# Performance work log

Hardware: AMD Instinct MI355X
Metric: run time of the kernel (lower is better)

## Reference

```python
import jax, jax.numpy as jnp
import numpy as np

HID = 128
HEADS = 8
HDIM = HID // HEADS
MLP = int(HID * 4.0)
N = 50000
E = 800000
EPS = 1e-6


def _ln(x):
    m = jnp.mean(x, axis=-1, keepdims=True)
    v = jnp.var(x, axis=-1, keepdims=True)
    return (x - m) / jnp.sqrt(v + EPS)


def _modulate(x, shift, scale):
    return x * (1 + scale) + shift


def setup_inputs() -> dict:
    key = jax.random.key(0)
    ks = jax.random.split(key, 12)
    s = lambda fan_in: 1.0 / np.sqrt(fan_in)
    return {
        "x": jax.random.normal(ks[0], (N, HID), dtype=jnp.float32),
        "edge_index": jax.random.randint(ks[1], (2, E), 0, N, dtype=jnp.int64),
        "c": jax.random.normal(ks[2], (N, HID), dtype=jnp.float32),
        "w_qkv": jax.random.normal(ks[3], (HID, 3 * HID), dtype=jnp.float32) * s(HID),
        "w_proj": jax.random.normal(ks[4], (HID, HID), dtype=jnp.float32) * s(HID),
        "b_proj": jnp.zeros((HID,), dtype=jnp.float32),
        "w_mlp1": jax.random.normal(ks[5], (HID, MLP), dtype=jnp.float32) * s(HID),
        "b_mlp1": jnp.zeros((MLP,), dtype=jnp.float32),
        "w_mlp2": jax.random.normal(ks[6], (MLP, HID), dtype=jnp.float32) * s(MLP),
        "b_mlp2": jnp.zeros((HID,), dtype=jnp.float32),
        "w_ada": jax.random.normal(ks[7], (HID, 6 * HID), dtype=jnp.float32) * s(HID),
        "b_ada": jnp.zeros((6 * HID,), dtype=jnp.float32),
    }


def _graph_attn(x, edge_index, w_qkv, w_proj, b_proj):
    n = x.shape[0]
    qkv = x @ w_qkv  # [N, 3*HID]
    q, k, v = jnp.split(qkv, 3, axis=-1)
    q = q.reshape(n, HEADS, HDIM)
    k = k.reshape(n, HEADS, HDIM)
    v = v.reshape(n, HEADS, HDIM)
    src = edge_index[0]  # j (source)
    dst = edge_index[1]  # i (destination / aggregation key)
    # per-edge attention score [E, HEADS]
    score = jnp.einsum('ehd,ehd->eh', q[dst], k[src]) / np.sqrt(HDIM)
    # segment softmax over destination node
    smax = jax.ops.segment_max(score, dst, num_segments=n)  # [N, H]
    ex = jnp.exp(score - smax[dst])
    den = jax.ops.segment_sum(ex, dst, num_segments=n)
    attn = ex / den[dst]  # [E, H]
    msg = v[src] * attn[:, :, None]  # [E, H, D]
    out = jax.ops.segment_sum(msg, dst, num_segments=n)  # [N, H, D]
    return out.reshape(n, HID) @ w_proj + b_proj


def reference(x, edge_index, c, w_qkv, w_proj, b_proj, w_mlp1, b_mlp1,
              w_mlp2, b_mlp2, w_ada, b_ada):
    mods = jax.nn.silu(c) @ w_ada + b_ada
    sh_msa, sc_msa, g_msa, sh_mlp, sc_mlp, g_mlp = jnp.split(mods, 6, axis=-1)
    x = x + g_msa * _graph_attn(_modulate(_ln(x), sh_msa, sc_msa),
                                edge_index, w_qkv, w_proj, b_proj)
    h = _modulate(_ln(x), sh_mlp, sc_mlp)
    h = jax.nn.gelu(h @ w_mlp1 + b_mlp1, approximate=True) @ w_mlp2 + b_mlp2
    return x + g_mlp * h
```

## Files before the change

kernel.cpp:

```cpp
#include <hip/hip_runtime.h>
#include <math.h>

#define N_NODES 50000
#define HIDD 128
#define HEADS 8
#define HDIM 16
#define NE 800000

using short8 = __attribute__((ext_vector_type(8))) short;
using f32x4 = __attribute__((ext_vector_type(4))) float;

__device__ __forceinline__ int load_idx(const void* ei, int is64, long long pos) {
  long long v = is64 ? ((const long long*)ei)[pos]
                     : (long long)((const int*)ei)[pos];
  unsigned uv = (unsigned)v;
  return (uv < N_NODES) ? (int)uv : 0;
}

__global__ void detect_kernel(const unsigned* __restrict__ ei_raw, int* flag) {
  __shared__ int any_nonzero;
  if (threadIdx.x == 0) any_nonzero = 0;
  __syncthreads();
  if (threadIdx.x < 128) {
    if (ei_raw[2 * threadIdx.x + 1] != 0u) atomicOr(&any_nonzero, 1);
  }
  __syncthreads();
  if (threadIdx.x == 0) *flag = any_nonzero ? 0 : 1;
}

__global__ __launch_bounds__(256) void probe_kernel(float* out, int n, float mb) {
  int i = blockIdx.x * 256 + threadIdx.x;
  if (i < n) out[i] = (i == 0) ? mb : 0.f;
}

struct ProNone {
  __device__ __forceinline__ float operator()(float v, int, int) const { return v; }
};
struct ProSilu {
  __device__ __forceinline__ float operator()(float v, int, int) const {
    return v / (1.f + __expf(-v));
  }
};
struct EpiNone {
  __device__ __forceinline__ float operator()(float a, int, int) const { return a; }
};
struct EpiBias {
  const float* b;
  __device__ __forceinline__ float operator()(float a, int, int c) const { return a + b[c]; }
};
struct EpiGelu {
  const float* b;
  __device__ __forceinline__ float operator()(float a, int, int c) const {
    float t = a + b[c];
    float u = 0.7978845608028654f * (t + 0.044715f * t * t * t);
    float au = fabsf(u);
    float e = __expf(2.f * au);
    float th = __builtin_copysignf(1.f - 2.f / (e + 1.f), u);
    return 0.5f * t * (1.f + th);
  }
};
struct EpiResGateB {
  const float* b;
  const float* xres;
  const unsigned short* gate;
  __device__ __forceinline__ float operator()(float a, int r, int c) const {
    float g = __uint_as_float((unsigned)gate[(size_t)r * 768 + c] << 16);
    return xres[(size_t)r * HIDD + c] + g * (a + b[c]);
  }
};

struct CvTab {
  int end[8];
  int src_sel[8];
  int src_off[8];
  int ldb[8];
  int n[8];
  int dst_off[8];
};
__global__ __launch_bounds__(256) void convert_all_kernel(
    const float* __restrict__ p0, const float* __restrict__ p1,
    const float* __restrict__ p2, const float* __restrict__ p3,
    const float* __restrict__ p4, CvTab t, int total,
    unsigned short* __restrict__ hi, unsigned short* __restrict__ lo) {
  int idx = blockIdx.x * 256 + threadIdx.x;
  if (idx >= total) return;
  int s = 0;
#pragma unroll
  for (int j = 0; j < 7; j++) s += (idx >= t.end[j]) ? 1 : 0;
  int local = idx - (s ? t.end[s - 1] : 0);
  int N = t.n[s];
  int k = (unsigned)local / (unsigned)N;
  int n = local - k * N;
  const float* B;
  int sel = t.src_sel[s];
  B = (sel == 0) ? p0 : (sel == 1) ? p1 : (sel == 2) ? p2 : (sel == 3) ? p3 : p4;
  float f = B[(size_t)k * t.ldb[s] + t.src_off[s] + n];
  unsigned u = __float_as_uint(f);
  unsigned short hs = (unsigned short)(u >> 16);
  float hf = __uint_as_float(u & 0xFFFF0000u);
  unsigned short ls = (unsigned short)(__float_as_uint(f - hf) >> 16);
  int lane = (((k >> 3) & 3) << 4) | (n & 15);
  int dst = t.dst_off[s] + (((k >> 5) * (N >> 4) + (n >> 4)) * 64 + lane) * 8 + (k & 7);
  hi[dst] = hs;
  lo[dst] = ls;
}

template <class Pro, class Epi, int OMODE = 0, int AMODE = 0>
__global__ __launch_bounds__(256) void gemm_direct(
    const void* __restrict__ Av, const void* __restrict__ Av2,
    const unsigned short* __restrict__ Bhi, const unsigned short* __restrict__ Blo,
    void* __restrict__ Cv, int M, int N, int K, Pro pro, Epi epi) {
  const int tid = threadIdx.x;
  const int lane = tid & 63;
  const int wv = tid >> 6;
  const int quad = lane >> 4;
  const int ln15 = lane & 15;
  const int mrow0 = blockIdx.x * 64 + wv * 16;
  const int arow = mrow0 + ln15;
  const int col0 = blockIdx.y * 128;
  const int Nt = N >> 4;
  const int ntbase = col0 >> 4;
  const bool aok = (arow < M);
  const int KB = K >> 5;
  float* C = (float*)Cv;

  f32x4 acc[8] = {};

  for (int kb = 0; kb < KB; kb++) {
    short8 ahi = {}, alo = {};
    if constexpr (AMODE == 0) {
      const float* A = (const float*)Av;
      float4 a0 = make_float4(0.f, 0.f, 0.f, 0.f), a1 = a0;
      if (aok) {
        const float* ap = A + (size_t)arow * K + kb * 32 + quad * 8;
        a0 = *(const float4*)ap;
        a1 = *(const float4*)(ap + 4);
        int cb = kb * 32 + quad * 8;
        a0.x = pro(a0.x, arow, cb + 0); a0.y = pro(a0.y, arow, cb + 1);
        a0.z = pro(a0.z, arow, cb + 2); a0.w = pro(a0.w, arow, cb + 3);
        a1.x = pro(a1.x, arow, cb + 4); a1.y = pro(a1.y, arow, cb + 5);
        a1.z = pro(a1.z, arow, cb + 6); a1.w = pro(a1.w, arow, cb + 7);
      }
      float f[8] = {a0.x, a0.y, a0.z, a0.w, a1.x, a1.y, a1.z, a1.w};
      union { unsigned u[4]; short8 v; } ch, cl;
#pragma unroll
      for (int e = 0; e < 4; e++) {
        unsigned u0 = __float_as_uint(f[2 * e]);
        unsigned u1 = __float_as_uint(f[2 * e + 1]);
        ch.u[e] = (u0 >> 16) | (u1 & 0xFFFF0000u);
        float h0 = __uint_as_float(u0 & 0xFFFF0000u);
        float h1 = __uint_as_float(u1 & 0xFFFF0000u);
        cl.u[e] = (__float_as_uint(f[2 * e] - h0) >> 16) |
                  (__float_as_uint(f[2 * e + 1] - h1) & 0xFFFF0000u);
      }
      ahi = ch.v;
      alo = cl.v;
    } else if constexpr (AMODE == 1) {
      if (aok)
        ahi = *(const short8*)((const unsigned short*)Av + (size_t)arow * K + kb * 32 + quad * 8);
    } else {
      if (aok) {
        size_t aoff = (size_t)arow * K + kb * 32 + quad * 8;
        ahi = *(const short8*)((const unsigned short*)Av + aoff);
        alo = *(const short8*)((const unsigned short*)Av2 + aoff);
      }
    }

    const unsigned short* bph = Bhi + ((size_t)(kb * Nt + ntbase) * 64 + lane) * 8;
    const unsigned short* bpl = Blo + ((size_t)(kb * Nt + ntbase) * 64 + lane) * 8;
#pragma unroll
    for (int nt = 0; nt < 8; nt++) {
      short8 bhi = *(const short8*)(bph + nt * 512);
      short8 blo = *(const short8*)(bpl + nt * 512);
      if constexpr (AMODE != 1)
        acc[nt] = __builtin_amdgcn_mfma_f32_16x16x32_bf16(alo, bhi, acc[nt], 0, 0, 0);
      acc[nt] = __builtin_amdgcn_mfma_f32_16x16x32_bf16(ahi, blo, acc[nt], 0, 0, 0);
      acc[nt] = __builtin_amdgcn_mfma_f32_16x16x32_bf16(ahi, bhi, acc[nt], 0, 0, 0);
    }
  }

#pragma unroll
  for (int nt = 0; nt < 8; nt++) {
    f32x4 a = acc[nt];
    int gc = col0 + nt * 16 + ln15;
#pragma unroll
    for (int r = 0; r < 4; r++) {
      int gr = mrow0 + quad * 4 + r;
      if (gr < M) {
        if constexpr (OMODE == 1) {
          float* crow = C + (size_t)gr * 256;
          if (gc < 128) {
            crow[gc] = a[r];
          } else {
            unsigned u = __float_as_uint(a[r]);
            unsigned rr = (u + 0x7FFFu + ((u >> 16) & 1u)) >> 16;
            unsigned short* kv = (unsigned short*)crow + 256;
            int c = gc - 128;
            int idx = (c < 128) ? (((c >> 2) << 3) + (c & 3))
                                : ((((c - 128) >> 2) << 3) + 4 + ((c - 128) & 3));
            kv[idx] = (unsigned short)rr;
          }
        } else if constexpr (OMODE == 2) {
          float v = epi(a[r], gr, gc);
          unsigned u = __float_as_uint(v);
          unsigned rr = (u + 0x7FFFu + ((u >> 16) & 1u)) >> 16;
          ((unsigned short*)Cv)[(size_t)gr * N + gc] = (unsigned short)rr;
        } else {
          C[(size_t)gr * N + gc] = epi(a[r], gr, gc);
        }
      }
    }
  }
}

__global__ __launch_bounds__(256) void ln_mod_kernel(
    const float* __restrict__ x, const unsigned* __restrict__ sa,
    unsigned* __restrict__ xh, unsigned* __restrict__ xl) {
  int wave = threadIdx.x >> 6;
  int lane = threadIdx.x & 63;
  int row = blockIdx.x * 4 + wave;
  if (row >= N_NODES) return;
  float2 v = *(const float2*)(x + (size_t)row * HIDD + lane * 2);
  float s = v.x + v.y;
  float sq = v.x * v.x + v.y * v.y;
#pragma unroll
  for (int o = 32; o >= 1; o >>= 1) {
    s += __shfl_xor(s, o);
    sq += __shfl_xor(sq, o);
  }
  float m = s * (1.f / 128.f);
  float var = sq * (1.f / 128.f) - m * m;
  float rs = rsqrtf(var + 1e-6f);
  unsigned shw = sa[(size_t)row * 384 + lane];
  unsigned scw = sa[(size_t)row * 384 + 64 + lane];
  float shx = __uint_as_float(shw << 16), shy = __uint_as_float(shw & 0xFFFF0000u);
  float scx = __uint_as_float(scw << 16), scy = __uint_as_float(scw & 0xFFFF0000u);
  float ox = (v.x - m) * rs * (1.f + scx) + shx;
  float oy = (v.y - m) * rs * (1.f + scy) + shy;
  unsigned ux = __float_as_uint(ox), uy = __float_as_uint(oy);
  unsigned hx = ux & 0xFFFF0000u, hy = uy & 0xFFFF0000u;
  unsigned lx = __float_as_uint(ox - __uint_as_float(hx));
  unsigned ly = __float_as_uint(oy - __uint_as_float(hy));
  xh[(size_t)row * 64 + lane] = (ux >> 16) | hy;
  xl[(size_t)row * 64 + lane] = (lx >> 16) | (ly & 0xFFFF0000u);
}

__global__ __launch_bounds__(256) void zero_int_kernel(int* p, int n) {
  int i = blockIdx.x * 256 + threadIdx.x;
  if (i < n) p[i] = 0;
}

__global__ __launch_bounds__(256) void hist_kernel(const void* __restrict__ ei,
                                                   const int* __restrict__ flag,
                                                   int* __restrict__ A) {
  int e = blockIdx.x * 256 + threadIdx.x;
  if (e >= NE) return;
  int dst = load_idx(ei, *flag, (long long)NE + e);
  atomicAdd(&A[dst + 1], 1);
}

__global__ __launch_bounds__(1024) void scan1_kernel(int* __restrict__ A, int n,
                                                     int* __restrict__ bsum) {
  __shared__ int buf[2][1024];
  int i = blockIdx.x * 1024 + threadIdx.x;
  int val = (i < n) ? A[i] : 0;
  int pb = 0;
  buf[0][threadIdx.x] = val;
  __syncthreads();
#pragma unroll
  for (int off = 1; off < 1024; off <<= 1) {
    int t = buf[pb][threadIdx.x];
    if ((int)threadIdx.x >= off) t += buf[pb][threadIdx.x - off];
    buf[pb ^ 1][threadIdx.x] = t;
    pb ^= 1;
    __syncthreads();
  }
  int incl = buf[pb][threadIdx.x];
  if (i < n) A[i] = incl;
  if (threadIdx.x == 1023) bsum[blockIdx.x] = incl;
}
__global__ void scan2_kernel(int* __restrict__ bsum, int nb) {
  int l = threadIdx.x;
  int v = (l < nb) ? bsum[l] : 0;
#pragma unroll
  for (int off = 1; off < 64; off <<= 1) {
    int t = __shfl_up(v, off);
    if (l >= off) v += t;
  }
  if (l < nb) bsum[l] = v;
}
__global__ __launch_bounds__(256) void scan3_kernel(int* __restrict__ A, int n,
                                                    const int* __restrict__ bsum) {
  int i = blockIdx.x * 256 + threadIdx.x;
  int b = i >> 10;
  if (i < n && b > 0) A[i] += bsum[b - 1];
}

__global__ __launch_bounds__(256) void scatter_kernel(const void* __restrict__ ei,
                                                      const int* __restrict__ flag,
                                                      int* __restrict__ A,
                                                      unsigned short* __restrict__ col) {
  int e = blockIdx.x * 256 + threadIdx.x;
  if (e >= NE) return;
  int is64 = *flag;
  int src = load_idx(ei, is64, e);
  int dst = load_idx(ei, is64, (long long)NE + e);
  int pos = atomicAdd(&A[dst], 1);
  col[pos] = (unsigned short)src;
}

__global__ __launch_bounds__(256) void node_attn_kernel(
    const int* __restrict__ A, const unsigned short* __restrict__ col,
    const float* __restrict__ qkv, float* __restrict__ attn) {
  int wave = threadIdx.x >> 6;
  int lane = threadIdx.x & 63;
  int half = lane >> 5;
  int l32 = lane & 31;
  int node = blockIdx.x * 4 + wave;
  if (node >= N_NODES) return;
  int start = (node == 0) ? 0 : A[node - 1];
  int end = A[node];
  int deg = end - start;

  float4 q = *(const float4*)(qkv + (size_t)node * 256 + l32 * 4);
  float l = 0.f;
  float4 acc = make_float4(0.f, 0.f, 0.f, 0.f);

  if (deg > 0) {
    int itc = (deg + 1) >> 1;
    int last = end - 1;
    const unsigned* qu = (const unsigned*)qkv;
    auto eidx = [&](int it) {
      int e = start + 2 * it + half;
      return (e <= last) ? e : last;
    };
    int i_cur = col[eidx(0)];
    int i_nxt = col[eidx(1)];
    uint4 kvc = *(const uint4*)(qu + (size_t)i_cur * 256 + 128 + 4 * l32);
    for (int it = 0; it < itc; it++) {
      uint4 kvn = kvc;
      if (it + 1 < itc)
        kvn = *(const uint4*)(qu + (size_t)i_nxt * 256 + 128 + 4 * l32);
      i_nxt = col[eidx(it + 2)];
      float kx = __uint_as_float(kvc.x << 16);
      float ky = __uint_as_float(kvc.x & 0xFFFF0000u);
      float kz = __uint_as_float(kvc.y << 16);
      float kw = __uint_as_float(kvc.y & 0xFFFF0000u);
      float s = q.x * kx + q.y * ky + q.z * kz + q.w * kw;
      s += __shfl_xor(s, 1);
      s += __shfl_xor(s, 2);
      s *= 0.25f;
      bool valid = (start + 2 * it + half) < end;
      float w = valid ? __expf(fminf(s, 60.f)) : 0.f;
      float vx = __uint_as_float(kvc.z << 16);
      float vy = __uint_as_float(kvc.z & 0xFFFF0000u);
      float vz = __uint_as_float(kvc.w << 16);
      float vw = __uint_as_float(kvc.w & 0xFFFF0000u);
      l += w;
      acc.x += w * vx;
      acc.y += w * vy;
      acc.z += w * vz;
      acc.w += w * vw;
      kvc = kvn;
    }
  }
  l += __shfl_xor(l, 32);
  acc.x += __shfl_xor(acc.x, 32);
  acc.y += __shfl_xor(acc.y, 32);
  acc.z += __shfl_xor(acc.z, 32);
  acc.w += __shfl_xor(acc.w, 32);
  float inv = (l > 0.f) ? 1.f / l : 0.f;
  if (half == 0) {
    float4 o = make_float4(acc.x * inv, acc.y * inv, acc.z * inv, acc.w * inv);
    *(float4*)(attn + (size_t)node * HIDD + l32 * 4) = o;
  }
}

extern "C" void kernel_launch(void* const* d_in, const int* in_sizes, int n_in,
                              void* d_out, int out_size, void* d_ws, size_t ws_size,
                              hipStream_t stream) {
  const float* x      = (const float*)d_in[0];
  const void*  ei     = d_in[1];
  const float* c      = (const float*)d_in[2];
  const float* w_qkv  = (const float*)d_in[3];
  const float* w_proj = (const float*)d_in[4];
  const float* b_proj = (const float*)d_in[5];
  const float* w_mlp1 = (const float*)d_in[6];
  const float* b_mlp1 = (const float*)d_in[7];
  const float* w_mlp2 = (const float*)d_in[8];
  const float* b_mlp2 = (const float*)d_in[9];
  const float* w_ada  = (const float*)d_in[10];
  const float* b_ada  = (const float*)d_in[11];
  float* out = (float*)d_out;

  const size_t NM = (size_t)N_NODES;
  unsigned short* ada = (unsigned short*)d_ws;
  float* buf1 = (float*)(ada + NM * 768);
  float* buf2 = buf1 + NM * 128;
  int*   Arow  = (int*)(buf2 + NM * 256);
  unsigned short* col = (unsigned short*)(Arow + 50048);
  int*   eflag = (int*)(col + NE);
  int*   bsum  = eflag + 8;
  unsigned short* Bhi = (unsigned short*)(bsum + 64);
  unsigned short* Blo = Bhi + 294912;
  unsigned* xh = (unsigned*)buf1;
  unsigned* xl = xh + NM * 64;
  float* attnb = buf1;
  float* qkv   = buf2;
  unsigned short* h1 = (unsigned short*)buf2;

  const int o_qkv = 0, o_ada = 49152, o_proj = 147456, o_mlp1 = 163840,
            o_mlp2 = 229376;
  const int cv_total = 294912;

  const size_t req_bytes = (NM * 768) * 4 + 50048 * 4 + NE * 2 + 32 + 256 +
                           (size_t)cv_total * 2 * 2;
  dim3 blk(256);
  if (ws_size < req_bytes) {
    probe_kernel<<<dim3((out_size + 255) / 256), blk, 0, stream>>>(
        out, out_size, (float)(ws_size >> 20));
    return;
  }

  const int MB = (N_NODES + 63) / 64;
  const int EB = (NE + 255) / 256;
  const int SB = (N_NODES + 1 + 1023) / 1024;

  detect_kernel<<<dim3(1), blk, 0, stream>>>((const unsigned*)ei, eflag);
  zero_int_kernel<<<dim3((N_NODES + 1 + 255) / 256), blk, 0, stream>>>(Arow, N_NODES + 1);
  hist_kernel<<<dim3(EB), blk, 0, stream>>>(ei, eflag, Arow);
  scan1_kernel<<<dim3(SB), dim3(1024), 0, stream>>>(Arow, N_NODES + 1, bsum);
  scan2_kernel<<<dim3(1), dim3(64), 0, stream>>>(bsum, SB);
  scan3_kernel<<<dim3((N_NODES + 1 + 255) / 256), blk, 0, stream>>>(Arow, N_NODES + 1, bsum);
  scatter_kernel<<<dim3(EB), blk, 0, stream>>>(ei, eflag, Arow, col);

  {
    CvTab t;
    int sel[8]     = { 0,      1,      2,      3,      4,      0, 0, 0 };
    int soff[8]    = { 0,      0,      0,      0,      0,      0, 0, 0 };
    int ldb[8]     = { 384,    768,    128,    512,    128,    1, 1, 1 };
    int nn[8]      = { 384,    768,    128,    512,    128,    1, 1, 1 };
    int doff[8]    = { o_qkv,  o_ada,  o_proj, o_mlp1, o_mlp2, 0, 0, 0 };
    int cnt[8]     = { 49152,  98304,  16384,  65536,  65536,  0, 0, 0 };
    int accum = 0;
    for (int s = 0; s < 8; s++) {
      accum += cnt[s];
      t.end[s] = accum; t.src_sel[s] = sel[s]; t.src_off[s] = soff[s];
      t.ldb[s] = ldb[s]; t.n[s] = nn[s]; t.dst_off[s] = doff[s];
    }
    convert_all_kernel<<<dim3((cv_total + 255) / 256), blk, 0, stream>>>(
        w_qkv, w_ada, w_proj, w_mlp1, w_mlp2, t, cv_total, Bhi, Blo);
  }

  gemm_direct<ProSilu, EpiBias, 2, 0><<<dim3(MB, 6), blk, 0, stream>>>(
      c, nullptr, Bhi + o_ada, Blo + o_ada, ada, N_NODES, 768, 128,
      ProSilu{}, EpiBias{b_ada});

  ln_mod_kernel<<<dim3((N_NODES + 3) / 4), blk, 0, stream>>>(
      x, (const unsigned*)ada, xh, xl);

  gemm_direct<ProNone, EpiNone, 1, 2><<<dim3(MB, 3), blk, 0, stream>>>(
      xh, xl, Bhi + o_qkv, Blo + o_qkv, qkv, N_NODES, 384, 128,
      ProNone{}, EpiNone{});

  node_attn_kernel<<<dim3((N_NODES + 3) / 4), blk, 0, stream>>>(Arow, col, qkv, attnb);

  gemm_direct<ProNone, EpiResGateB, 0, 0><<<dim3(MB, 1), blk, 0, stream>>>(
      attnb, nullptr, Bhi + o_proj, Blo + o_proj, out, N_NODES, 128, 128,
      ProNone{}, EpiResGateB{b_proj, x, ada + 256});

  ln_mod_kernel<<<dim3((N_NODES + 3) / 4), blk, 0, stream>>>(
      out, (const unsigned*)(ada + 384), xh, xl);

  gemm_direct<ProNone, EpiGelu, 2, 2><<<dim3(MB, 4), blk, 0, stream>>>(
      xh, xl, Bhi + o_mlp1, Blo + o_mlp1, h1, N_NODES, 512, 128,
      ProNone{}, EpiGelu{b_mlp1});

  gemm_direct<ProNone, EpiResGateB, 0, 1><<<dim3(MB, 1), blk, 0, stream>>>(
      h1, nullptr, Bhi + o_mlp2, Blo + o_mlp2, out, N_NODES, 128, 512,
      ProNone{}, EpiResGateB{b_mlp2, out, ada + 640});
}
```

Measured before the change: 550.8 us.

## Fuse LayerNorm-modulate into GEMM prologue and loop all column groups per block

The standalone ln_mod kernels are removed. The QKV and MLP1 GEMMs now read x, compute row mean and variance with cross-lane shuffles, apply the shift and scale from the ada buffer, and split the result into bf16 hi/lo fragments in registers. Each GEMM block also keeps its A fragments resident and loops over all column groups (NG) instead of launching one block per 128-column slice, so A is loaded and converted once per row tile. This removes the xh/xl intermediate round trip and the repeated A reads, at the cost of more registers, fewer blocks (MB instead of MB×6) and longer serial work per block.

```diff
diff --git a/kernel.cpp b/kernel.cpp
--- a/kernel.cpp
+++ b/kernel.cpp
@@ -105,80 +105,60 @@
   lo[dst] = ls;
 }
 
-template <class Pro, class Epi, int OMODE = 0, int AMODE = 0>
-__global__ __launch_bounds__(256) void gemm_direct(
-    const void* __restrict__ Av, const void* __restrict__ Av2,
-    const unsigned short* __restrict__ Bhi, const unsigned short* __restrict__ Blo,
-    void* __restrict__ Cv, int M, int N, int K, Pro pro, Epi epi) {
-  const int tid = threadIdx.x;
-  const int lane = tid & 63;
-  const int wv = tid >> 6;
-  const int quad = lane >> 4;
-  const int ln15 = lane & 15;
-  const int mrow0 = blockIdx.x * 64 + wv * 16;
-  const int arow = mrow0 + ln15;
-  const int col0 = blockIdx.y * 128;
-  const int Nt = N >> 4;
-  const int ntbase = col0 >> 4;
-  const bool aok = (arow < M);
-  const int KB = K >> 5;
+__device__ __forceinline__ void split8(const float f[8], short8& ahi, short8& alo) {
+  union { unsigned u[4]; short8 v; } ch, cl;
+#pragma unroll
+  for (int e = 0; e < 4; e++) {
+    unsigned u0 = __float_as_uint(f[2 * e]);
+    unsigned u1 = __float_as_uint(f[2 * e + 1]);
+    ch.u[e] = (u0 >> 16) | (u1 & 0xFFFF0000u);
+    float h0 = __uint_as_float(u0 & 0xFFFF0000u);
+    float h1 = __uint_as_float(u1 & 0xFFFF0000u);
+    cl.u[e] = (__float_as_uint(f[2 * e] - h0) >> 16) |
+              (__float_as_uint(f[2 * e + 1] - h1) & 0xFFFF0000u);
+  }
+  ahi = ch.v;
+  alo = cl.v;
+}
+
+template <class Pro, int AMODE>
+__device__ __forceinline__ void load_a_frag(
+    const void* __restrict__ Av, const void* __restrict__ Av2, int arow, int K,
+    int kb, int quad, bool aok, Pro pro, short8& ahi, short8& alo) {
+  ahi = {};
+  alo = {};
+  if constexpr (AMODE == 0) {
+    const float* A = (const float*)Av;
+    float4 a0 = make_float4(0.f, 0.f, 0.f, 0.f), a1 = a0;
+    if (aok) {
+      const float* ap = A + (size_t)arow * K + kb * 32 + quad * 8;
+      a0 = *(const float4*)ap;
+      a1 = *(const float4*)(ap + 4);
+      int cb = kb * 32 + quad * 8;
+      a0.x = pro(a0.x, arow, cb + 0); a0.y = pro(a0.y, arow, cb + 1);
+      a0.z = pro(a0.z, arow, cb + 2); a0.w = pro(a0.w, arow, cb + 3);
+      a1.x = pro(a1.x, arow, cb + 4); a1.y = pro(a1.y, arow, cb + 5);
+      a1.z = pro(a1.z, arow, cb + 6); a1.w = pro(a1.w, arow, cb + 7);
+    }
+    float f[8] = {a0.x, a0.y, a0.z, a0.w, a1.x, a1.y, a1.z, a1.w};
+    split8(f, ahi, alo);
+  } else if constexpr (AMODE == 1) {
+    if (aok)
+      ahi = *(const short8*)((const unsigned short*)Av + (size_t)arow * K + kb * 32 + quad * 8);
+  } else {
+    if (aok) {
+      size_t aoff = (size_t)arow * K + kb * 32 + quad * 8;
+      ahi = *(const short8*)((const unsigned short*)Av + aoff);
+      alo = *(const short8*)((const unsigned short*)Av2 + aoff);
+    }
+  }
+}
+
+template <class Epi, int OMODE>
+__device__ __forceinline__ void store_tiles(
+    const f32x4* acc, void* __restrict__ Cv, int M, int N, int mrow0, int col0,
+    int quad, int ln15, Epi epi) {
   float* C = (float*)Cv;
-
-  f32x4 acc[8] = {};
-
-  for (int kb = 0; kb < KB; kb++) {
-    short8 ahi = {}, alo = {};
-    if constexpr (AMODE == 0) {
-      const float* A = (const float*)Av;
-      float4 a0 = make_float4(0.f, 0.f, 0.f, 0.f), a1 = a0;
-      if (aok) {
-        const float* ap = A + (size_t)arow * K + kb * 32 + quad * 8;
-        a0 = *(const float4*)ap;
-        a1 = *(const float4*)(ap + 4);
-        int cb = kb * 32 + quad * 8;
-        a0.x = pro(a0.x, arow, cb + 0); a0.y = pro(a0.y, arow, cb + 1);
-        a0.z = pro(a0.z, arow, cb + 2); a0.w = pro(a0.w, arow, cb + 3);
-        a1.x = pro(a1.x, arow, cb + 4); a1.y = pro(a1.y, arow, cb + 5);
-        a1.z = pro(a1.z, arow, cb + 6); a1.w = pro(a1.w, arow, cb + 7);
-      }
-      float f[8] = {a0.x, a0.y, a0.z, a0.w, a1.x, a1.y, a1.z, a1.w};
-      union { unsigned u[4]; short8 v; } ch, cl;
-#pragma unroll
-      for (int e = 0; e < 4; e++) {
-        unsigned u0 = __float_as_uint(f[2 * e]);
-        unsigned u1 = __float_as_uint(f[2 * e + 1]);
-        ch.u[e] = (u0 >> 16) | (u1 & 0xFFFF0000u);
-        float h0 = __uint_as_float(u0 & 0xFFFF0000u);
-        float h1 = __uint_as_float(u1 & 0xFFFF0000u);
-        cl.u[e] = (__float_as_uint(f[2 * e] - h0) >> 16) |
-                  (__float_as_uint(f[2 * e + 1] - h1) & 0xFFFF0000u);
-      }
-      ahi = ch.v;
-      alo = cl.v;
-    } else if constexpr (AMODE == 1) {
-      if (aok)
-        ahi = *(const short8*)((const unsigned short*)Av + (size_t)arow * K + kb * 32 + quad * 8);
-    } else {
-      if (aok) {
-        size_t aoff = (size_t)arow * K + kb * 32 + quad * 8;
-        ahi = *(const short8*)((const unsigned short*)Av + aoff);
-        alo = *(const short8*)((const unsigned short*)Av2 + aoff);
-      }
-    }
-
-    const unsigned short* bph = Bhi + ((size_t)(kb * Nt + ntbase) * 64 + lane) * 8;
-    const unsigned short* bpl = Blo + ((size_t)(kb * Nt + ntbase) * 64 + lane) * 8;
-#pragma unroll
-    for (int nt = 0; nt < 8; nt++) {
-      short8 bhi = *(const short8*)(bph + nt * 512);
-      short8 blo = *(const short8*)(bpl + nt * 512);
-      if constexpr (AMODE != 1)
-        acc[nt] = __builtin_amdgcn_mfma_f32_16x16x32_bf16(alo, bhi, acc[nt], 0, 0, 0);
-      acc[nt] = __builtin_amdgcn_mfma_f32_16x16x32_bf16(ahi, blo, acc[nt], 0, 0, 0);
-      acc[nt] = __builtin_amdgcn_mfma_f32_16x16x32_bf16(ahi, bhi, acc[nt], 0, 0, 0);
-    }
-  }
-
 #pragma unroll
   for (int nt = 0; nt < 8; nt++) {
     f32x4 a = acc[nt];
@@ -213,36 +193,112 @@
   }
 }
 
-__global__ __launch_bounds__(256) void ln_mod_kernel(
-    const float* __restrict__ x, const unsigned* __restrict__ sa,
-    unsigned* __restrict__ xh, unsigned* __restrict__ xl) {
-  int wave = threadIdx.x >> 6;
-  int lane = threadIdx.x & 63;
-  int row = blockIdx.x * 4 + wave;
-  if (row >= N_NODES) return;
-  float2 v = *(const float2*)(x + (size_t)row * HIDD + lane * 2);
-  float s = v.x + v.y;
-  float sq = v.x * v.x + v.y * v.y;
-#pragma unroll
-  for (int o = 32; o >= 1; o >>= 1) {
-    s += __shfl_xor(s, o);
-    sq += __shfl_xor(sq, o);
-  }
-  float m = s * (1.f / 128.f);
-  float var = sq * (1.f / 128.f) - m * m;
-  float rs = rsqrtf(var + 1e-6f);
-  unsigned shw = sa[(size_t)row * 384 + lane];
-  unsigned scw = sa[(size_t)row * 384 + 64 + lane];
-  float shx = __uint_as_float(shw << 16), shy = __uint_as_float(shw & 0xFFFF0000u);
-  float scx = __uint_as_float(scw << 16), scy = __uint_as_float(scw & 0xFFFF0000u);
-  float ox = (v.x - m) * rs * (1.f + scx) + shx;
-  float oy = (v.y - m) * rs * (1.f + scy) + shy;
-  unsigned ux = __float_as_uint(ox), uy = __float_as_uint(oy);
-  unsigned hx = ux & 0xFFFF0000u, hy = uy & 0xFFFF0000u;
-  unsigned lx = __float_as_uint(ox - __uint_as_float(hx));
-  unsigned ly = __float_as_uint(oy - __uint_as_float(hy));
-  xh[(size_t)row * 64 + lane] = (ux >> 16) | hy;
-  xl[(size_t)row * 64 + lane] = (lx >> 16) | (ly & 0xFFFF0000u);
+template <class Pro, class Epi, int OMODE = 0, int AMODE = 0, int NG = 1>
+__global__ __launch_bounds__(256) void gemm_direct(
+    const void* __restrict__ Av, const void* __restrict__ Av2,
+    const unsigned short* __restrict__ Bhi, const unsigned short* __restrict__ Blo,
+    void* __restrict__ Cv, int M, int N, int K, Pro pro, Epi epi) {
+  const int tid = threadIdx.x;
+  const int lane = tid & 63;
+  const int wv = tid >> 6;
+  const int quad = lane >> 4;
+  const int ln15 = lane & 15;
+  const int mrow0 = blockIdx.x * 64 + wv * 16;
+  const int arow = mrow0 + ln15;
+  const int Nt = N >> 4;
+  const bool aok = (arow < M);
+
+  if constexpr (NG > 1) {
+    short8 AH[4], AL[4];
+    if constexpr (AMODE == 3) {
+      const float* X = (const float*)Av;
+      const unsigned short* adap = (const unsigned short*)Av2;
+      float xf[4][8];
+      float s = 0.f, sq = 0.f;
+#pragma unroll
+      for (int kb = 0; kb < 4; kb++) {
+        float4 a0 = make_float4(0.f, 0.f, 0.f, 0.f), a1 = a0;
+        if (aok) {
+          const float* ap = X + (size_t)arow * 128 + kb * 32 + quad * 8;
+          a0 = *(const float4*)ap;
+          a1 = *(const float4*)(ap + 4);
+        }
+        xf[kb][0] = a0.x; xf[kb][1] = a0.y; xf[kb][2] = a0.z; xf[kb][3] = a0.w;
+        xf[kb][4] = a1.x; xf[kb][5] = a1.y; xf[kb][6] = a1.z; xf[kb][7] = a1.w;
+#pragma unroll
+        for (int e = 0; e < 8; e++) {
+          s += xf[kb][e];
+          sq += xf[kb][e] * xf[kb][e];
+        }
+      }
+      s += __shfl_xor(s, 16); s += __shfl_xor(s, 32);
+      sq += __shfl_xor(sq, 16); sq += __shfl_xor(sq, 32);
+      float m = s * (1.f / 128.f);
+      float var = sq * (1.f / 128.f) - m * m;
+      float rs = rsqrtf(var + 1e-6f);
+#pragma unroll
+      for (int kb = 0; kb < 4; kb++) {
+        short8 shw = {}, scw = {};
+        if (aok) {
+          const unsigned short* rp = adap + (size_t)arow * 768 + kb * 32 + quad * 8;
+          shw = *(const short8*)rp;
+          scw = *(const short8*)(rp + 128);
+        }
+        float f[8];
+#pragma unroll
+        for (int e = 0; e < 8; e++) {
+          float sh = __uint_as_float((unsigned)(unsigned short)shw[e] << 16);
+          float sc = __uint_as_float((unsigned)(unsigned short)scw[e] << 16);
+          f[e] = (xf[kb][e] - m) * rs * (1.f + sc) + sh;
+        }
+        split8(f, AH[kb], AL[kb]);
+      }
+    } else {
+#pragma unroll
+      for (int kb = 0; kb < 4; kb++)
+        load_a_frag<Pro, AMODE>(Av, Av2, arow, K, kb, quad, aok, pro, AH[kb], AL[kb]);
+    }
+
+    for (int g = 0; g < NG; g++) {
+      f32x4 acc[8] = {};
+#pragma unroll
+      for (int kb = 0; kb < 4; kb++) {
+        const unsigned short* bph = Bhi + ((size_t)(kb * Nt + g * 8) * 64 + lane) * 8;
+        const unsigned short* bpl = Blo + ((size_t)(kb * Nt + g * 8) * 64 + lane) * 8;
+#pragma unroll
+        for (int nt = 0; nt < 8; nt++) {
+          short8 bhi = *(const short8*)(bph + nt * 512);
+          short8 blo = *(const short8*)(bpl + nt * 512);
+          if constexpr (AMODE != 1)
+            acc[nt] = __builtin_amdgcn_mfma_f32_16x16x32_bf16(AL[kb], bhi, acc[nt], 0, 0, 0);
+          acc[nt] = __builtin_amdgcn_mfma_f32_16x16x32_bf16(AH[kb], blo, acc[nt], 0, 0, 0);
+          acc[nt] = __builtin_amdgcn_mfma_f32_16x16x32_bf16(AH[kb], bhi, acc[nt], 0, 0, 0);
+        }
+      }
+      store_tiles<Epi, OMODE>(acc, Cv, M, N, mrow0, g * 128, quad, ln15, epi);
+    }
+  } else {
+    const int col0 = blockIdx.y * 128;
+    const int ntbase = col0 >> 4;
+    const int KB = K >> 5;
+    f32x4 acc[8] = {};
+    for (int kb = 0; kb < KB; kb++) {
+      short8 ahi, alo;
+      load_a_frag<Pro, AMODE>(Av, Av2, arow, K, kb, quad, aok, pro, ahi, alo);
+      const unsigned short* bph = Bhi + ((size_t)(kb * Nt + ntbase) * 64 + lane) * 8;
+      const unsigned short* bpl = Blo + ((size_t)(kb * Nt + ntbase) * 64 + lane) * 8;
+#pragma unroll
+      for (int nt = 0; nt < 8; nt++) {
+        short8 bhi = *(const short8*)(bph + nt * 512);
+        short8 blo = *(const short8*)(bpl + nt * 512);
+        if constexpr (AMODE != 1)
+          acc[nt] = __builtin_amdgcn_mfma_f32_16x16x32_bf16(alo, bhi, acc[nt], 0, 0, 0);
+        acc[nt] = __builtin_amdgcn_mfma_f32_16x16x32_bf16(ahi, blo, acc[nt], 0, 0, 0);
+        acc[nt] = __builtin_amdgcn_mfma_f32_16x16x32_bf16(ahi, bhi, acc[nt], 0, 0, 0);
+      }
+    }
+    store_tiles<Epi, OMODE>(acc, Cv, M, N, mrow0, col0, quad, ln15, epi);
+  }
 }
 
 __global__ __launch_bounds__(256) void zero_int_kernel(int* p, int n) {
@@ -403,8 +459,6 @@
   int*   bsum  = eflag + 8;
   unsigned short* Bhi = (unsigned short*)(bsum + 64);
   unsigned short* Blo = Bhi + 294912;
-  unsigned* xh = (unsigned*)buf1;
-  unsigned* xl = xh + NM * 64;
   float* attnb = buf1;
   float* qkv   = buf2;
   unsigned short* h1 = (unsigned short*)buf2;
@@ -452,31 +506,25 @@
         w_qkv, w_ada, w_proj, w_mlp1, w_mlp2, t, cv_total, Bhi, Blo);
   }
 
-  gemm_direct<ProSilu, EpiBias, 2, 0><<<dim3(MB, 6), blk, 0, stream>>>(
+  gemm_direct<ProSilu, EpiBias, 2, 0, 6><<<dim3(MB, 1), blk, 0, stream>>>(
       c, nullptr, Bhi + o_ada, Blo + o_ada, ada, N_NODES, 768, 128,
       ProSilu{}, EpiBias{b_ada});
 
-  ln_mod_kernel<<<dim3((N_NODES + 3) / 4), blk, 0, stream>>>(
-      x, (const unsigned*)ada, xh, xl);
-
-  gemm_direct<ProNone, EpiNone, 1, 2><<<dim3(MB, 3), blk, 0, stream>>>(
-      xh, xl, Bhi + o_qkv, Blo + o_qkv, qkv, N_NODES, 384, 128,
+  gemm_direct<ProNone, EpiNone, 1, 3, 3><<<dim3(MB, 1), blk, 0, stream>>>(
+      x, ada, Bhi + o_qkv, Blo + o_qkv, qkv, N_NODES, 384, 128,
       ProNone{}, EpiNone{});
 
   node_attn_kernel<<<dim3((N_NODES + 3) / 4), blk, 0, stream>>>(Arow, col, qkv, attnb);
 
-  gemm_direct<ProNone, EpiResGateB, 0, 0><<<dim3(MB, 1), blk, 0, stream>>>(
+  gemm_direct<ProNone, EpiResGateB, 0, 0, 1><<<dim3(MB, 1), blk, 0, stream>>>(
       attnb, nullptr, Bhi + o_proj, Blo + o_proj, out, N_NODES, 128, 128,
       ProNone{}, EpiResGateB{b_proj, x, ada + 256});
 
-  ln_mod_kernel<<<dim3((N_NODES + 3) / 4), blk, 0, stream>>>(
-      out, (const unsigned*)(ada + 384), xh, xl);
-
-  gemm_direct<ProNone, EpiGelu, 2, 2><<<dim3(MB, 4), blk, 0, stream>>>(
-      xh, xl, Bhi + o_mlp1, Blo + o_mlp1, h1, N_NODES, 512, 128,
+  gemm_direct<ProNone, EpiGelu, 2, 3, 4><<<dim3(MB, 1), blk, 0, stream>>>(
+      out, ada + 384, Bhi + o_mlp1, Blo + o_mlp1, h1, N_NODES, 512, 128,
       ProNone{}, EpiGelu{b_mlp1});
 
-  gemm_direct<ProNone, EpiResGateB, 0, 1><<<dim3(MB, 1), blk, 0, stream>>>(
+  gemm_direct<ProNone, EpiResGateB, 0, 1, 1><<<dim3(MB, 1), blk, 0, stream>>>(
       h1, nullptr, Bhi + o_mlp2, Blo + o_mlp2, out, N_NODES, 128, 512,
       ProNone{}, EpiResGateB{b_mlp2, out, ada + 640});
 }
```

Measured after the change: 560.4 us. About the same (+1.7%).
